# Kernel tuning notes

Measured on AMD Instinct MI355X. Metric: run time of the kernel, lower is better.

The kernel has to match this reference:

```python
import jax, jax.numpy as jnp
import numpy as np

B, T, C = 4, 2048, 2048
H = 16
D = C // H  # 128


def setup_inputs() -> dict:
    key = jax.random.key(0)
    ks = jax.random.split(key, 9)
    s = 0.02
    return {
        "x": jax.random.normal(ks[0], (B, T, C), dtype=jnp.float32),
        "wq": jax.random.normal(ks[1], (C, C), dtype=jnp.float32) * s,
        "bq": jax.random.normal(ks[2], (C,), dtype=jnp.float32) * s,
        "wk": jax.random.normal(ks[3], (C, C), dtype=jnp.float32) * s,
        "bk": jax.random.normal(ks[4], (C,), dtype=jnp.float32) * s,
        "wv": jax.random.normal(ks[5], (C, C), dtype=jnp.float32) * s,
        "bv": jax.random.normal(ks[6], (C,), dtype=jnp.float32) * s,
        "wo": jax.random.normal(ks[7], (C, C), dtype=jnp.float32) * s,
        "bo": jax.random.normal(ks[8], (C,), dtype=jnp.float32) * s,
    }


def reference(x, wq, bq, wk, bk, wv, bv, wo, bo):
    Bz, Tz, Cz = x.shape
    # projections (torch Linear: x @ W^T + b)
    q = (x @ wq.T + bq).reshape(Bz, Tz, H, D).transpose(0, 2, 1, 3)  # [B,H,T,D]
    k = (x @ wk.T + bk).reshape(Bz, Tz, H, D).transpose(0, 2, 1, 3)
    v = (x @ wv.T + bv).reshape(Bz, Tz, H, D).transpose(0, 2, 1, 3)
    scale = 1.0 / jnp.sqrt(jnp.float32(D))
    scores = jnp.einsum("bhqd,bhkd->bhqk", q, k) * scale  # [B,H,T,T]
    causal = jnp.tril(jnp.ones((Tz, Tz), dtype=bool))
    scores = jnp.where(causal, scores, jnp.float32(-jnp.inf))
    att = jax.nn.softmax(scores, axis=-1)
    out = jnp.einsum("bhqk,bhkd->bhqd", att, v)  # [B,H,T,D]
    out = out.transpose(0, 2, 1, 3).reshape(Bz, Tz, Cz)
    out = out @ wo.T + bo
    return out
```

## Files before the change

kernel.cpp:

```cpp
#include <hip/hip_runtime.h>
#include <hip/hip_bf16.h>

typedef float  f32x4  __attribute__((ext_vector_type(4)));
typedef __bf16 bf16x8 __attribute__((ext_vector_type(8)));
typedef __bf16 bf16x4 __attribute__((ext_vector_type(4)));

#define Bz 4
#define Tz 2048
#define Cz 2048
#define Hh 16
#define Dd 128
#define Mm 8192

__device__ __forceinline__ void gload_lds16(const __bf16* g, __bf16* l) {
  __builtin_amdgcn_global_load_lds(
      (const __attribute__((address_space(1))) void*)g,
      (__attribute__((address_space(3))) void*)l, 16, 0, 0);
}

__global__ __launch_bounds__(256)
void cvt_bf16(const float* __restrict__ in, __bf16* __restrict__ out, int n8) {
  int i = blockIdx.x * 256 + threadIdx.x;
  if (i >= n8) return;
  size_t base = (size_t)i * 8;
  f32x4 a = *(const f32x4*)(in + base);
  f32x4 b = *(const f32x4*)(in + base + 4);
  bf16x8 o;
  o[0]=(__bf16)a[0]; o[1]=(__bf16)a[1]; o[2]=(__bf16)a[2]; o[3]=(__bf16)a[3];
  o[4]=(__bf16)b[0]; o[5]=(__bf16)b[1]; o[6]=(__bf16)b[2]; o[7]=(__bf16)b[3];
  *(bf16x8*)(out + base) = o;
}

template<int MODE>
__global__ __launch_bounds__(256, 2)
void gemm_bt(const __bf16* __restrict__ A, const __bf16* __restrict__ W,
             const float* __restrict__ bias, void* __restrict__ Out,
             int K, float scale)
{
  __shared__ __bf16 As[128 * 64];
  __shared__ __bf16 Bs[128 * 64];

  const int tid  = threadIdx.x;
  const int lane = tid & 63;
  const int wave = tid >> 6;
  const int wm = wave >> 1, wn = wave & 1;
  const int g  = lane >> 4;
  const int lr = lane & 15;
  const int row0 = blockIdx.x * 128;
  const int col0 = blockIdx.y * 128;

  const int srow = lane >> 3;
  const int sblk = lane & 7;

  f32x4 acc[4][4] = {};

  for (int kt = 0; kt < K; kt += 64) {
    __syncthreads();
    #pragma unroll
    for (int p = 0; p < 4; ++p) {
      const int rb = p * 32 + wave * 8;
      const int r  = rb + srow;
      const int cb = sblk ^ (r & 7);
      gload_lds16(A + (size_t)(row0 + r) * K + kt + cb * 8, As + rb * 64);
      gload_lds16(W + (size_t)(col0 + r) * K + kt + cb * 8, Bs + rb * 64);
    }
    __syncthreads();
    #pragma unroll
    for (int kk = 0; kk < 2; ++kk) {
      bf16x8 af[4], bfr[4];
      #pragma unroll
      for (int i = 0; i < 4; ++i) {
        const int ar = wm * 64 + i * 16 + lr;
        af[i]  = *(const bf16x8*)(As + ar * 64 + ((((kk<<2)|g) ^ (ar & 7)) << 3));
        const int br = wn * 64 + i * 16 + lr;
        bfr[i] = *(const bf16x8*)(Bs + br * 64 + ((((kk<<2)|g) ^ (br & 7)) << 3));
      }
      #pragma unroll
      for (int i = 0; i < 4; ++i)
        #pragma unroll
        for (int j = 0; j < 4; ++j)
          acc[i][j] = __builtin_amdgcn_mfma_f32_16x16x32_bf16(af[i], bfr[j], acc[i][j], 0, 0, 0);
    }
  }

  #pragma unroll
  for (int j = 0; j < 4; ++j) {
    const int col = col0 + wn * 64 + j * 16 + lr;
    const float bv = bias[col];
    #pragma unroll
    for (int i = 0; i < 4; ++i) {
      if (MODE == 2) {
        const int row = row0 + wm * 64 + i * 16 + g * 4;
        const int b = row >> 11, t = row & (Tz - 1);
        const int h = col >> 7,  d = col & (Dd - 1);
        bf16x4 v4;
        #pragma unroll
        for (int r = 0; r < 4; ++r) v4[r] = (__bf16)(acc[i][j][r] + bv);
        *(bf16x4*)((__bf16*)Out + ((size_t)(b * Hh + h) * Dd + d) * Tz + t) = v4;
      } else {
        #pragma unroll
        for (int r = 0; r < 4; ++r) {
          const int row = row0 + wm * 64 + i * 16 + g * 4 + r;
          const float v = acc[i][j][r] + bv;
          if (MODE == 0) {
            const int b = row >> 11, t = row & (Tz - 1);
            const int h = col >> 7,  d = col & (Dd - 1);
            ((__bf16*)Out)[((size_t)(b * Hh + h) * Tz + t) * Dd + d] = (__bf16)(v * scale);
          } else {
            ((float*)Out)[(size_t)row * Cz + col] = v;
          }
        }
      }
    }
  }
}

__global__ __launch_bounds__(256, 2)
void attn_fwd(const __bf16* __restrict__ Q, const __bf16* __restrict__ Kg,
              const __bf16* __restrict__ Vt, __bf16* __restrict__ O)
{
  __shared__ __bf16 Ks[2][64 * 128];
  __shared__ __bf16 Vs[2][128 * 64];
  __shared__ __bf16 Ps[4][32 * 64];

  const int tid  = threadIdx.x;
  const int lane = tid & 63;
  const int wave = tid >> 6;
  const int g  = lane >> 4;
  const int lr = lane & 15;
  const int pair = blockIdx.y;
  const int b = pair >> 4, h = pair & 15;

  const __bf16* Qp = Q  + (size_t)pair * Tz * Dd;
  const __bf16* Kp = Kg + (size_t)pair * Tz * Dd;
  const __bf16* Vp = Vt + (size_t)pair * Dd * Tz;

  #define STAGE_KV(kv0_, buf_)                                                  \
    {                                                                           \
      const int kv0s = (kv0_);                                                  \
      _Pragma("unroll")                                                         \
      for (int p = 0; p < 4; ++p) {                                             \
        const int r  = p * 16 + wave * 4 + (lane >> 4);                         \
        const int cb = (lane & 15) ^ (r & 7);                                   \
        gload_lds16(Kp + (size_t)(kv0s + r) * Dd + cb * 8,                      \
                    &Ks[buf_][p * 2048 + wave * 512]);                          \
        const int d  = p * 32 + wave * 8 + (lane >> 3);                         \
        const int cv = (lane & 7) ^ (d & 7);                                    \
        gload_lds16(Vp + (size_t)d * Tz + kv0s + cv * 8,                        \
                    &Vs[buf_][p * 2048 + wave * 512]);                          \
      }                                                                         \
    }

  for (int pass = 0; pass < 2; ++pass) {
    const int qt  = pass == 0 ? (15 - (int)blockIdx.x) : (int)blockIdx.x;
    const int qw0 = qt * 128 + wave * 32;

    bf16x8 qf[2][4];
    #pragma unroll
    for (int im = 0; im < 2; ++im)
      #pragma unroll
      for (int ks = 0; ks < 4; ++ks)
        qf[im][ks] = *(const bf16x8*)(Qp + (size_t)(qw0 + im*16 + lr) * Dd + ks*32 + g*8);

    f32x4 oacc[2][8] = {};
    float mrow[2], lsum[2];
    mrow[0] = mrow[1] = -1e30f;
    lsum[0] = lsum[1] = 0.f;

    const int ntiles = 2 * qt + 2;

    STAGE_KV(0, 0);
    __syncthreads();

    for (int kt = 0; kt < ntiles; ++kt) {
      const int cur = kt & 1;
      const int kv0 = kt * 64;
      if (kt + 1 < ntiles) STAGE_KV((kt + 1) * 64, cur ^ 1);

      if (kv0 <= qw0 + 31) {
        f32x4 sacc[2][4] = {};
        __builtin_amdgcn_s_setprio(1);
        #pragma unroll
        for (int ks = 0; ks < 4; ++ks) {
          bf16x8 kf[4];
          #pragma unroll
          for (int in = 0; in < 4; ++in) {
            const int r = in*16 + lr;
            kf[in] = *(const bf16x8*)(&Ks[cur][r * 128 + ((((ks<<2)|g) ^ (r & 7)) << 3)]);
          }
          #pragma unroll
          for (int im = 0; im < 2; ++im)
            #pragma unroll
            for (int in = 0; in < 4; ++in)
              sacc[im][in] = __builtin_amdgcn_mfma_f32_16x16x32_bf16(kf[in], qf[im][ks], sacc[im][in], 0, 0, 0);
        }
        __builtin_amdgcn_s_setprio(0);

        if (kv0 + 63 > qw0) {
          #pragma unroll
          for (int im = 0; im < 2; ++im) {
            const int q = qw0 + im*16 + lr;
            #pragma unroll
            for (int in = 0; in < 4; ++in)
              #pragma unroll
              for (int r = 0; r < 4; ++r) {
                const int kv = kv0 + in*16 + g*4 + r;
                if (kv > q) sacc[im][in][r] = -3e38f;
              }
          }
        }

        #pragma unroll
        for (int im = 0; im < 2; ++im) {
          float m = fmaxf(fmaxf(sacc[im][0][0], sacc[im][0][1]),
                          fmaxf(sacc[im][0][2], sacc[im][0][3]));
          #pragma unroll
          for (int in = 1; in < 4; ++in)
            m = fmaxf(m, fmaxf(fmaxf(sacc[im][in][0], sacc[im][in][1]),
                               fmaxf(sacc[im][in][2], sacc[im][in][3])));
          m = fmaxf(m, __shfl_xor(m, 16));
          m = fmaxf(m, __shfl_xor(m, 32));

          const bool need = m > mrow[im] + 11.54f;
          if (__any(need)) {
            const float mn   = need ? m : mrow[im];
            const float corr = __builtin_amdgcn_exp2f(mrow[im] - mn);
            mrow[im] = mn;
            lsum[im] *= corr;
            const int sb = 20 * g;
            const float c0 = __shfl(corr, sb + 0);
            const float c1 = __shfl(corr, sb + 1);
            const float c2 = __shfl(corr, sb + 2);
            const float c3 = __shfl(corr, sb + 3);
            #pragma unroll
            for (int dn = 0; dn < 8; ++dn) {
              oacc[im][dn][0] *= c0; oacc[im][dn][1] *= c1;
              oacc[im][dn][2] *= c2; oacc[im][dn][3] *= c3;
            }
          }

          float rs = 0.f;
          const int prow = im*16 + lr;
          #pragma unroll
          for (int in = 0; in < 4; ++in) {
            const float p0 = __builtin_amdgcn_exp2f(sacc[im][in][0] - mrow[im]);
            const float p1 = __builtin_amdgcn_exp2f(sacc[im][in][1] - mrow[im]);
            const float p2 = __builtin_amdgcn_exp2f(sacc[im][in][2] - mrow[im]);
            const float p3 = __builtin_amdgcn_exp2f(sacc[im][in][3] - mrow[im]);
            rs += (p0 + p1) + (p2 + p3);
            bf16x4 q4;
            q4[0] = (__bf16)p0; q4[1] = (__bf16)p1;
            q4[2] = (__bf16)p2; q4[3] = (__bf16)p3;
            const int bs = (in*4 + g) ^ ((prow & 3) << 2);
            *(bf16x4*)(&Ps[wave][prow * 64 + bs * 4]) = q4;
          }
          rs += __shfl_xor(rs, 16);
          rs += __shfl_xor(rs, 32);
          lsum[im] += rs;
        }

        __builtin_amdgcn_s_setprio(1);
        #pragma unroll
        for (int kk = 0; kk < 2; ++kk) {
          bf16x8 pa[2];
          #pragma unroll
          for (int im = 0; im < 2; ++im) {
            const int prow = im*16 + lr;
            const int bs = (kk*8 + 2*g) ^ ((prow & 3) << 2);
            pa[im] = *(const bf16x8*)(&Ps[wave][prow * 64 + bs * 4]);
          }
          #pragma unroll
          for (int dn = 0; dn < 8; ++dn) {
            const int d = dn*16 + lr;
            bf16x8 vb = *(const bf16x8*)(&Vs[cur][d * 64 + ((((kk<<2)|g) ^ (d & 7)) << 3)]);
            #pragma unroll
            for (int im = 0; im < 2; ++im)
              oacc[im][dn] = __builtin_amdgcn_mfma_f32_16x16x32_bf16(pa[im], vb, oacc[im][dn], 0, 0, 0);
          }
        }
        __builtin_amdgcn_s_setprio(0);
      }
      __syncthreads();
    }

    #pragma unroll
    for (int im = 0; im < 2; ++im) {
      const float inv = 1.0f / lsum[im];
      const int sb = 20 * g;
      const float i0 = __shfl(inv, sb + 0);
      const float i1 = __shfl(inv, sb + 1);
      const float i2 = __shfl(inv, sb + 2);
      const float i3 = __shfl(inv, sb + 3);
      #pragma unroll
      for (int dn = 0; dn < 8; ++dn) {
        const int qrow = qw0 + im*16 + g*4;
        const int d    = h * Dd + dn*16 + lr;
        O[((size_t)(b * Tz + qrow + 0)) * Cz + d] = (__bf16)(oacc[im][dn][0] * i0);
        O[((size_t)(b * Tz + qrow + 1)) * Cz + d] = (__bf16)(oacc[im][dn][1] * i1);
        O[((size_t)(b * Tz + qrow + 2)) * Cz + d] = (__bf16)(oacc[im][dn][2] * i2);
        O[((size_t)(b * Tz + qrow + 3)) * Cz + d] = (__bf16)(oacc[im][dn][3] * i3);
      }
    }
  }
  #undef STAGE_KV
}

extern "C" void kernel_launch(void* const* d_in, const int* in_sizes, int n_in,
                              void* d_out, int out_size, void* d_ws, size_t ws_size,
                              hipStream_t stream) {
  const float* x  = (const float*)d_in[0];
  const float* wq = (const float*)d_in[1];
  const float* bq = (const float*)d_in[2];
  const float* wk = (const float*)d_in[3];
  const float* bk = (const float*)d_in[4];
  const float* wv = (const float*)d_in[5];
  const float* bv = (const float*)d_in[6];
  const float* wo = (const float*)d_in[7];
  const float* bo = (const float*)d_in[8];
  float* out = (float*)d_out;

  char* w = (char*)d_ws;
  __bf16* xb   = (__bf16*)w; w += (size_t)Mm * Cz * 2;
  __bf16* wbuf = (__bf16*)w; w += (size_t)Cz * Cz * 2;
  __bf16* qb   = (__bf16*)w; w += (size_t)Mm * Cz * 2;
  __bf16* kb   = (__bf16*)w; w += (size_t)Mm * Cz * 2;
  __bf16* vbuf = (__bf16*)w; w += (size_t)Mm * Cz * 2;
  if (ws_size < (size_t)(w - (char*)d_ws)) return;

  const int nx8 = Mm * Cz / 8;
  const int nw8 = Cz * Cz / 8;
  dim3 ggrid(Mm / 128, Cz / 128);
  const float qscale = 0.12752551286084110f;

  cvt_bf16<<<nx8 / 256, 256, 0, stream>>>(x, xb, nx8);

  cvt_bf16<<<nw8 / 256, 256, 0, stream>>>(wq, wbuf, nw8);
  gemm_bt<0><<<ggrid, 256, 0, stream>>>(xb, wbuf, bq, qb, Cz, qscale);

  cvt_bf16<<<nw8 / 256, 256, 0, stream>>>(wk, wbuf, nw8);
  gemm_bt<0><<<ggrid, 256, 0, stream>>>(xb, wbuf, bk, kb, Cz, 1.0f);

  cvt_bf16<<<nw8 / 256, 256, 0, stream>>>(wv, wbuf, nw8);
  gemm_bt<2><<<ggrid, 256, 0, stream>>>(xb, wbuf, bv, vbuf, Cz, 1.0f);

  __bf16* ob = xb;
  attn_fwd<<<dim3(8, Bz * Hh), 256, 0, stream>>>(qb, kb, vbuf, ob);

  cvt_bf16<<<nw8 / 256, 256, 0, stream>>>(wo, wbuf, nw8);
  gemm_bt<1><<<ggrid, 256, 0, stream>>>(ob, wbuf, bo, out, Cz, 1.0f);
}
```

Before: 412.3 us.

## Enlarge GEMM tiles to 256x256 with double-buffered LDS prefetch pipeline

Reworks the projection GEMM from 128x128 tiles with 4 waves to 256x256 tiles with 8 waves. It double-buffers the LDS stages so the next K-slice is loaded while MFMAs run on the current one, and interleaves loads with compute in four phases using raw barriers and setprio. The aim is higher arithmetic intensity and hidden global-load latency. The cost is 128KB of LDS per block and more accumulator registers, which limits occupancy. The grid also shrinks to 256 blocks, about one wave of blocks on the device.

```diff
diff --git a/kernel.cpp b/kernel.cpp
--- a/kernel.cpp
+++ b/kernel.cpp
@@ -32,65 +32,93 @@
 }
 
 template<int MODE>
-__global__ __launch_bounds__(256, 2)
+__global__ __launch_bounds__(512, 2)
 void gemm_bt(const __bf16* __restrict__ A, const __bf16* __restrict__ W,
              const float* __restrict__ bias, void* __restrict__ Out,
              int K, float scale)
 {
-  __shared__ __bf16 As[128 * 64];
-  __shared__ __bf16 Bs[128 * 64];
+  __shared__ __bf16 As[2][256 * 64];
+  __shared__ __bf16 Bs[2][256 * 64];
 
   const int tid  = threadIdx.x;
   const int lane = tid & 63;
   const int wave = tid >> 6;
-  const int wm = wave >> 1, wn = wave & 1;
+  const int wm = wave >> 2, wn = wave & 3;
   const int g  = lane >> 4;
   const int lr = lane & 15;
-  const int row0 = blockIdx.x * 128;
-  const int col0 = blockIdx.y * 128;
-
-  const int srow = lane >> 3;
-  const int sblk = lane & 7;
-
-  f32x4 acc[4][4] = {};
-
-  for (int kt = 0; kt < K; kt += 64) {
-    __syncthreads();
+  const int row0 = blockIdx.x * 256;
+  const int col0 = blockIdx.y * 256;
+
+  #define STG(MAT, PTR, base0, kofs, buf)                                \
+    _Pragma("unroll")                                                    \
+    for (int q = 0; q < 4; ++q) {                                        \
+      const int r  = q * 64 + (tid >> 3);                                \
+      const int cb = (tid & 7) ^ (r & 7);                                \
+      gload_lds16(PTR + (size_t)(base0 + r) * K + (kofs) + cb * 8,       \
+                  &MAT[buf][(q * 64 + wave * 8) * 64]);                  \
+    }
+
+  f32x4 acc[8][4] = {};
+
+  STG(As, A, row0, 0, 0);
+  STG(Bs, W, col0, 0, 0);
+  asm volatile("s_waitcnt vmcnt(0)" ::: "memory");
+  asm volatile("s_barrier" ::: "memory");
+
+  const int NT = K >> 6;
+  bf16x8 bfr[4][2];
+  for (int kt = 0; kt < NT; ++kt) {
+    const int d  = kt & 1;
+    const bool pf = (kt + 1 < NT);
+    const int kn = (kt + 1) << 6;
+
     #pragma unroll
     for (int p = 0; p < 4; ++p) {
-      const int rb = p * 32 + wave * 8;
-      const int r  = rb + srow;
-      const int cb = sblk ^ (r & 7);
-      gload_lds16(A + (size_t)(row0 + r) * K + kt + cb * 8, As + rb * 64);
-      gload_lds16(W + (size_t)(col0 + r) * K + kt + cb * 8, Bs + rb * 64);
-    }
-    __syncthreads();
-    #pragma unroll
-    for (int kk = 0; kk < 2; ++kk) {
-      bf16x8 af[4], bfr[4];
+      if (p == 0) {
+        #pragma unroll
+        for (int n = 0; n < 4; ++n)
+          #pragma unroll
+          for (int kk = 0; kk < 2; ++kk) {
+            const int br = wn * 64 + n * 16 + lr;
+            bfr[n][kk] = *(const bf16x8*)(&Bs[d][br * 64 + ((((kk << 2) | g) ^ (br & 7)) << 3)]);
+          }
+      }
+      bf16x8 af[2][2];
       #pragma unroll
-      for (int i = 0; i < 4; ++i) {
-        const int ar = wm * 64 + i * 16 + lr;
-        af[i]  = *(const bf16x8*)(As + ar * 64 + ((((kk<<2)|g) ^ (ar & 7)) << 3));
-        const int br = wn * 64 + i * 16 + lr;
-        bfr[i] = *(const bf16x8*)(Bs + br * 64 + ((((kk<<2)|g) ^ (br & 7)) << 3));
-      }
+      for (int mf = 0; mf < 2; ++mf)
+        #pragma unroll
+        for (int kk = 0; kk < 2; ++kk) {
+          const int ar = wm * 128 + (p * 2 + mf) * 16 + lr;
+          af[mf][kk] = *(const bf16x8*)(&As[d][ar * 64 + ((((kk << 2) | g) ^ (ar & 7)) << 3)]);
+        }
+      if (pf && p == 0) STG(As, A, row0, kn, d ^ 1);
+      if (pf && p == 1) STG(Bs, W, col0, kn, d ^ 1);
+
+      asm volatile("s_barrier" ::: "memory");
+      __builtin_amdgcn_s_setprio(1);
       #pragma unroll
-      for (int i = 0; i < 4; ++i)
-        #pragma unroll
-        for (int j = 0; j < 4; ++j)
-          acc[i][j] = __builtin_amdgcn_mfma_f32_16x16x32_bf16(af[i], bfr[j], acc[i][j], 0, 0, 0);
+      for (int kk = 0; kk < 2; ++kk)
+        #pragma unroll
+        for (int mf = 0; mf < 2; ++mf)
+          #pragma unroll
+          for (int n = 0; n < 4; ++n)
+            acc[p * 2 + mf][n] = __builtin_amdgcn_mfma_f32_16x16x32_bf16(
+                af[mf][kk], bfr[n][kk], acc[p * 2 + mf][n], 0, 0, 0);
+      __builtin_amdgcn_s_setprio(0);
+      if (p == 3) asm volatile("s_waitcnt vmcnt(0)" ::: "memory");
+      asm volatile("s_barrier" ::: "memory");
     }
   }
+  #undef STG
 
   #pragma unroll
   for (int j = 0; j < 4; ++j) {
     const int col = col0 + wn * 64 + j * 16 + lr;
     const float bv = bias[col];
     #pragma unroll
-    for (int i = 0; i < 4; ++i) {
+    for (int i = 0; i < 8; ++i) {
       if (MODE == 2) {
-        const int row = row0 + wm * 64 + i * 16 + g * 4;
+        const int row = row0 + wm * 128 + i * 16 + g * 4;
         const int b = row >> 11, t = row & (Tz - 1);
         const int h = col >> 7,  d = col & (Dd - 1);
         bf16x4 v4;
@@ -100,7 +128,7 @@
       } else {
         #pragma unroll
         for (int r = 0; r < 4; ++r) {
-          const int row = row0 + wm * 64 + i * 16 + g * 4 + r;
+          const int row = row0 + wm * 128 + i * 16 + g * 4 + r;
           const float v = acc[i][j][r] + bv;
           if (MODE == 0) {
             const int b = row >> 11, t = row & (Tz - 1);
@@ -329,23 +357,23 @@
 
   const int nx8 = Mm * Cz / 8;
   const int nw8 = Cz * Cz / 8;
-  dim3 ggrid(Mm / 128, Cz / 128);
+  dim3 ggrid(Mm / 256, Cz / 256);
   const float qscale = 0.12752551286084110f;
 
   cvt_bf16<<<nx8 / 256, 256, 0, stream>>>(x, xb, nx8);
 
   cvt_bf16<<<nw8 / 256, 256, 0, stream>>>(wq, wbuf, nw8);
-  gemm_bt<0><<<ggrid, 256, 0, stream>>>(xb, wbuf, bq, qb, Cz, qscale);
+  gemm_bt<0><<<ggrid, 512, 0, stream>>>(xb, wbuf, bq, qb, Cz, qscale);
 
   cvt_bf16<<<nw8 / 256, 256, 0, stream>>>(wk, wbuf, nw8);
-  gemm_bt<0><<<ggrid, 256, 0, stream>>>(xb, wbuf, bk, kb, Cz, 1.0f);
+  gemm_bt<0><<<ggrid, 512, 0, stream>>>(xb, wbuf, bk, kb, Cz, 1.0f);
 
   cvt_bf16<<<nw8 / 256, 256, 0, stream>>>(wv, wbuf, nw8);
-  gemm_bt<2><<<ggrid, 256, 0, stream>>>(xb, wbuf, bv, vbuf, Cz, 1.0f);
+  gemm_bt<2><<<ggrid, 512, 0, stream>>>(xb, wbuf, bv, vbuf, Cz, 1.0f);
 
   __bf16* ob = xb;
   attn_fwd<<<dim3(8, Bz * Hh), 256, 0, stream>>>(qb, kb, vbuf, ob);
 
   cvt_bf16<<<nw8 / 256, 256, 0, stream>>>(wo, wbuf, nw8);
-  gemm_bt<1><<<ggrid, 256, 0, stream>>>(ob, wbuf, bo, out, Cz, 1.0f);
-}
+  gemm_bt<1><<<ggrid, 512, 0, stream>>>(ob, wbuf, bo, out, Cz, 1.0f);
+}
```

Result: slower. 423.0 us (+2.6%).
